# Kernel optimization log

Measured on AMD Instinct MI355X. Metric: run time of the kernel, lower is better.

Reference implementation:

```python
import jax, jax.numpy as jnp
import numpy as np

SPATIAL_SHAPES = ((100, 167), (50, 84), (25, 42), (13, 21))
NUM_HEADS = 8
NUM_LEVELS = 4
NUM_POINTS = 4
EMBED_DIM = 256
LV = sum(h * w for h, w in SPATIAL_SHAPES)  # 22223


def bilinear_sample(img, grid):
    """torch.F.grid_sample(mode='bilinear', padding_mode='zeros', align_corners=False).
    img: (B, D, H, W); grid: (B, Lq, P, 2) with xy in [-1, 1]. Returns (B, D, Lq, P)."""
    B, D, H, W = img.shape
    x = (grid[..., 0] + 1.0) * 0.5 * W - 0.5  # (B, Lq, P)
    y = (grid[..., 1] + 1.0) * 0.5 * H - 0.5
    x0 = jnp.floor(x)
    y0 = jnp.floor(y)
    wx1 = x - x0
    wy1 = y - y0
    wx0 = 1.0 - wx1
    wy0 = 1.0 - wy1

    def gather(ix, iy):
        valid = ((ix >= 0) & (ix <= W - 1) & (iy >= 0) & (iy <= H - 1)).astype(img.dtype)
        ixc = jnp.clip(ix, 0, W - 1).astype(jnp.int32)
        iyc = jnp.clip(iy, 0, H - 1).astype(jnp.int32)

        def g(img_b, ixb, iyb, vb):
            return img_b[:, iyb, ixb] * vb[None]  # (D, Lq, P)

        return jax.vmap(g)(img, ixc, iyc, valid)  # (B, D, Lq, P)

    v00 = gather(x0, y0)
    v01 = gather(x0 + 1, y0)
    v10 = gather(x0, y0 + 1)
    v11 = gather(x0 + 1, y0 + 1)
    w00 = (wy0 * wx0)[:, None]
    w01 = (wy0 * wx1)[:, None]
    w10 = (wy1 * wx0)[:, None]
    w11 = (wy1 * wx1)[:, None]
    return v00 * w00 + v01 * w01 + v10 * w10 + v11 * w11


def deform_attn(query, ref_points, value, W_off, b_off, W_attn, b_attn, W_val, b_val, W_out, b_out):
    N, Lq, C = query.shape
    D = C // NUM_HEADS
    off = (query @ W_off + b_off).reshape(N, Lq, NUM_HEADS, NUM_LEVELS, NUM_POINTS, 2)
    attn = jax.nn.softmax((query @ W_attn + b_attn).reshape(N, Lq, NUM_HEADS, NUM_LEVELS * NUM_POINTS), axis=-1)
    attn = attn.reshape(N, Lq, NUM_HEADS, NUM_LEVELS, NUM_POINTS)
    ref_cxcy = ref_points[:, :, None, :, None, :2]
    ref_wh = ref_points[:, :, None, :, None, 2:]
    loc = ref_cxcy + off / NUM_POINTS * ref_wh * 0.5
    grids = 2.0 * loc - 1.0  # (N, Lq, nh, L, P, 2)

    v = value @ W_val + b_val  # (N, Lv, C)
    sampled = []
    start = 0
    for lvl, (H, W) in enumerate(SPATIAL_SHAPES):
        v_l = v[:, start:start + H * W]  # (N, HW, C)
        start += H * W
        v_l = v_l.transpose(0, 2, 1).reshape(N * NUM_HEADS, D, H, W)
        g_l = grids[:, :, :, lvl].transpose(0, 2, 1, 3, 4).reshape(N * NUM_HEADS, Lq, NUM_POINTS, 2)
        sampled.append(bilinear_sample(v_l, g_l))  # (N*nh, D, Lq, P)
    sampled = jnp.concatenate(sampled, axis=-1)  # (N*nh, D, Lq, L*P)

    attn_r = attn.transpose(0, 2, 1, 3, 4).reshape(N * NUM_HEADS, 1, Lq, NUM_LEVELS * NUM_POINTS)
    out = (sampled * attn_r).sum(-1)  # (N*nh, D, Lq)
    out = out.reshape(N, C, Lq).transpose(0, 2, 1)
    return out @ W_out + b_out


def setup_inputs() -> dict:
    key = jax.random.key(0)
    ks = jax.random.split(key, 8)
    N, Lq, C = 1, LV, EMBED_DIM
    s = 0.02
    return {
        "query": jax.random.normal(ks[0], (N, Lq, C), jnp.float32),
        "ref_points": jax.random.uniform(ks[1], (N, Lq, NUM_LEVELS, 4), jnp.float32),
        "value": jax.random.normal(ks[2], (N, LV, C), jnp.float32),
        "W_off": jax.random.normal(ks[3], (C, NUM_HEADS * NUM_LEVELS * NUM_POINTS * 2), jnp.float32) * s,
        "b_off": jnp.zeros((NUM_HEADS * NUM_LEVELS * NUM_POINTS * 2,), jnp.float32),
        "W_attn": jax.random.normal(ks[4], (C, NUM_HEADS * NUM_LEVELS * NUM_POINTS), jnp.float32) * s,
        "b_attn": jnp.zeros((NUM_HEADS * NUM_LEVELS * NUM_POINTS,), jnp.float32),
        "W_val": jax.random.normal(ks[5], (C, C), jnp.float32) * s,
        "b_val": jnp.zeros((C,), jnp.float32),
        "W_out": jax.random.normal(ks[6], (C, C), jnp.float32) * s,
        "b_out": jnp.zeros((C,), jnp.float32),
    }


def reference(query, ref_points, value, W_off, b_off, W_attn, b_attn, W_val, b_val, W_out, b_out):
    return deform_attn(query, ref_points, value, W_off, b_off, W_attn, b_attn, W_val, b_val, W_out, b_out)
```

## Files before the change

### kernel.cpp

```cpp
#include <hip/hip_runtime.h>
#include <math.h>

#define LQ 22223
#define NH 8
#define NL 4
#define NP 4
#define CDIM 256
#define MBLK 348
#define NBV  (176 * 8)
#define NBOA (264 * 8)

typedef __attribute__((ext_vector_type(8))) short short8;
typedef __attribute__((ext_vector_type(4))) float f32x4;

__device__ __forceinline__ ushort f2bf(float f) {
    union { float f; unsigned u; } c; c.f = f;
    unsigned u = c.u;
    return (ushort)((u + 0x7fffu + ((u >> 16) & 1u)) >> 16);
}
__device__ __forceinline__ float bflo(unsigned u) {
    union { unsigned u; float f; } c; c.u = u << 16; return c.f;
}
__device__ __forceinline__ float bfhi(unsigned u) {
    union { unsigned u; float f; } c; c.u = u & 0xffff0000u; return c.f;
}

__global__ __launch_bounds__(256) void convert_wt(
    const float* __restrict__ Wv, const float* __restrict__ Wo,
    const float* __restrict__ Wu, const float* __restrict__ Wa,
    const float* __restrict__ bo, const float* __restrict__ ba,
    ushort* __restrict__ Tv, ushort* __restrict__ Toa,
    ushort* __restrict__ Tu, float* __restrict__ bcat)
{
    int idx = blockIdx.x * 256 + threadIdx.x;
    if (idx >= 229376) {
        int b = idx - 229376;
        if (b < 384) bcat[b] = (b < 256) ? bo[b] : ba[b - 256];
        return;
    }
    const float* W; ushort* T; int N; int local;
    if      (idx < 65536)  { W = Wv; T = Tv;          N = 256; local = idx; }
    else if (idx < 131072) { W = Wo; T = Toa;         N = 256; local = idx - 65536; }
    else if (idx < 196608) { W = Wu; T = Tu;          N = 256; local = idx - 131072; }
    else                   { W = Wa; T = Toa + 65536; N = 128; local = idx - 196608; }
    int k = local & 255;
    int n = local >> 8;
    T[n * 256 + k] = f2bf(W[k * N + n]);
}

__global__ __launch_bounds__(256, 5) void gemm_dual(
    const float* __restrict__ value, const ushort* __restrict__ Wtv,
    const float* __restrict__ bv, ushort* __restrict__ Cv,
    const float* __restrict__ query, const ushort* __restrict__ Wtoa,
    const float* __restrict__ boa, float* __restrict__ Coa)
{
    const int K = 256;
    __shared__ ushort As[2][64 * 40];
    __shared__ ushort Bs[2][64 * 40];

    int b = blockIdx.x;
    const float* A; const ushort* Bt; const float* bias;
    int N, bx, by; bool isv;
    const int xcd = b & 7;
    if (b < NBV) {
        isv = true;  A = value; Bt = Wtv;  bias = bv;  N = 256;
        const int j = b >> 3;
        bx = j & 3;  by = xcd + 8 * (j >> 2);
    } else {
        isv = false; A = query; Bt = Wtoa; bias = boa; N = 384;
        const int j = (b - NBV) >> 3;
        bx = j % 6;  by = xcd + 8 * (j / 6);
    }
    if (by >= MBLK) return;

    const int tid = threadIdx.x;
    const int w = tid >> 6;
    const int l = tid & 63;
    const int bm = by * 64;
    const int bn = bx * 64;

    const int r = tid >> 2;
    const int c = tid & 3;

    const int m_l  = (w << 4) + (l & 15);
    const int koff = (l >> 4) << 3;

    const bool arow_ok = (bm + r) < LQ;
    const float*  Ap = A  + (size_t)(bm + r) * K + c * 8;
    const ushort* Bp = Bt + (size_t)(bn + r) * K + c * 8;

    auto ldA = [&](int k0) -> short8 {
        short8 av = {0, 0, 0, 0, 0, 0, 0, 0};
        if (arow_ok) {
            const float4 f0 = *reinterpret_cast<const float4*>(Ap + k0);
            const float4 f1 = *reinterpret_cast<const float4*>(Ap + k0 + 4);
            av[0] = (short)f2bf(f0.x); av[1] = (short)f2bf(f0.y);
            av[2] = (short)f2bf(f0.z); av[3] = (short)f2bf(f0.w);
            av[4] = (short)f2bf(f1.x); av[5] = (short)f2bf(f1.y);
            av[6] = (short)f2bf(f1.z); av[7] = (short)f2bf(f1.w);
        }
        return av;
    };

    short8 av = ldA(0);
    short8 bvv = *reinterpret_cast<const short8*>(Bp);
    *reinterpret_cast<short8*>(&As[0][r * 40 + c * 8]) = av;
    *reinterpret_cast<short8*>(&Bs[0][r * 40 + c * 8]) = bvv;

    f32x4 acc[4] = {};

    #pragma unroll
    for (int k = 0; k < 8; ++k) {
        __syncthreads();
        if (k < 7) {
            av  = ldA((k + 1) * 32);
            bvv = *reinterpret_cast<const short8*>(Bp + (k + 1) * 32);
        }
        const int cur = k & 1;
        const short8 af = *reinterpret_cast<const short8*>(&As[cur][m_l * 40 + koff]);
        #pragma unroll
        for (int t = 0; t < 4; ++t) {
            const short8 bf = *reinterpret_cast<const short8*>(
                &Bs[cur][(t * 16 + (l & 15)) * 40 + koff]);
            acc[t] = __builtin_amdgcn_mfma_f32_16x16x32_bf16(af, bf, acc[t], 0, 0, 0);
        }
        if (k < 7) {
            const int nxt = cur ^ 1;
            *reinterpret_cast<short8*>(&As[nxt][r * 40 + c * 8]) = av;
            *reinterpret_cast<short8*>(&Bs[nxt][r * 40 + c * 8]) = bvv;
        }
    }

    const int row0 = bm + (w << 4) + ((l >> 4) << 2);
    #pragma unroll
    for (int t = 0; t < 4; ++t) {
        const int col = bn + t * 16 + (l & 15);
        const float bs = bias[col];
        #pragma unroll
        for (int i = 0; i < 4; ++i) {
            const int row = row0 + i;
            if (row < LQ) {
                const float o = acc[t][i] + bs;
                if (isv) {
                    const int head = col >> 5;
                    const int ch   = col & 31;
                    Cv[(size_t)head * ((size_t)LQ * 32) + (size_t)row * 32 + ch] = f2bf(o);
                } else {
                    Coa[(size_t)row * 384 + col] = o;
                }
            }
        }
    }
}

__global__ __launch_bounds__(256, 5) void gemm_out(
    const ushort* __restrict__ A, const ushort* __restrict__ Bt,
    const float* __restrict__ bias, float* __restrict__ C)
{
    const int K = 256, N = 256;
    __shared__ ushort As[2][64 * 40];
    __shared__ ushort Bs[2][64 * 40];

    const int b = blockIdx.x;
    const int xcd = b & 7;
    const int j = b >> 3;
    const int bx = j & 3;
    const int by = xcd + 8 * (j >> 2);
    if (by >= MBLK) return;

    const int tid = threadIdx.x;
    const int w = tid >> 6;
    const int l = tid & 63;
    const int bm = by * 64;
    const int bn = bx * 64;

    const int r = tid >> 2;
    const int c = tid & 3;

    const int m_l  = (w << 4) + (l & 15);
    const int koff = (l >> 4) << 3;

    const bool arow_ok = (bm + r) < LQ;
    const ushort* Ap = A  + (size_t)(bm + r) * K + c * 8;
    const ushort* Bp = Bt + (size_t)(bn + r) * K + c * 8;

    auto ldA = [&](int k0) -> short8 {
        short8 av = {0, 0, 0, 0, 0, 0, 0, 0};
        if (arow_ok) av = *reinterpret_cast<const short8*>(Ap + k0);
        return av;
    };

    short8 av = ldA(0);
    short8 bvv = *reinterpret_cast<const short8*>(Bp);
    *reinterpret_cast<short8*>(&As[0][r * 40 + c * 8]) = av;
    *reinterpret_cast<short8*>(&Bs[0][r * 40 + c * 8]) = bvv;

    f32x4 acc[4] = {};

    #pragma unroll
    for (int k = 0; k < 8; ++k) {
        __syncthreads();
        if (k < 7) {
            av  = ldA((k + 1) * 32);
            bvv = *reinterpret_cast<const short8*>(Bp + (k + 1) * 32);
        }
        const int cur = k & 1;
        const short8 af = *reinterpret_cast<const short8*>(&As[cur][m_l * 40 + koff]);
        #pragma unroll
        for (int t = 0; t < 4; ++t) {
            const short8 bf = *reinterpret_cast<const short8*>(
                &Bs[cur][(t * 16 + (l & 15)) * 40 + koff]);
            acc[t] = __builtin_amdgcn_mfma_f32_16x16x32_bf16(af, bf, acc[t], 0, 0, 0);
        }
        if (k < 7) {
            const int nxt = cur ^ 1;
            *reinterpret_cast<short8*>(&As[nxt][r * 40 + c * 8]) = av;
            *reinterpret_cast<short8*>(&Bs[nxt][r * 40 + c * 8]) = bvv;
        }
    }

    const int row0 = bm + (w << 4) + ((l >> 4) << 2);
    #pragma unroll
    for (int t = 0; t < 4; ++t) {
        const int col = bn + t * 16 + (l & 15);
        const float bs = bias[col];
        #pragma unroll
        for (int i = 0; i < 4; ++i) {
            const int row = row0 + i;
            if (row < LQ) C[(size_t)row * N + col] = acc[t][i] + bs;
        }
    }
}

__global__ __launch_bounds__(256) void softmax16(float* __restrict__ offattn, int rows)
{
    const int r = blockIdx.x * 256 + threadIdx.x;
    if (r >= rows) return;
    const int q = r >> 3;
    const int h = r & 7;
    float4* p = reinterpret_cast<float4*>(offattn + (size_t)q * 384 + 256 + h * 16);
    float v[16];
    #pragma unroll
    for (int i = 0; i < 4; ++i) {
        const float4 f = p[i];
        v[i * 4 + 0] = f.x; v[i * 4 + 1] = f.y; v[i * 4 + 2] = f.z; v[i * 4 + 3] = f.w;
    }
    float m = v[0];
    #pragma unroll
    for (int i = 1; i < 16; ++i) m = fmaxf(m, v[i]);
    float s = 0.f;
    #pragma unroll
    for (int i = 0; i < 16; ++i) { v[i] = expf(v[i] - m); s += v[i]; }
    const float inv = 1.f / s;
    #pragma unroll
    for (int i = 0; i < 4; ++i)
        p[i] = make_float4(v[i * 4 + 0] * inv, v[i * 4 + 1] * inv,
                           v[i * 4 + 2] * inv, v[i * 4 + 3] * inv);
}

__global__ __launch_bounds__(256, 4) void msda_sample(
    const ushort* __restrict__ v, const float* __restrict__ offattn,
    const float* __restrict__ ref, ushort* __restrict__ outp)
{
    __shared__ int4   s_off[512];
    __shared__ float4 s_wts[512];

    const int h = blockIdx.x & 7;
    const int qbase = (blockIdx.x >> 3) * 64;
    const int tid = threadIdx.x;

    const int Hs[4] = {100, 50, 25, 13};
    const int Ws[4] = {167, 84, 42, 21};
    const int starts[4] = {0, 16700, 20900, 21950};
    const int h32 = h * 32;

    const int qi = tid >> 2;
    const int dg = tid & 3;
    const int q2 = qbase + qi;
    const int d8 = dg * 8;
    const ushort* vh = v + (size_t)h * ((size_t)LQ * 32) + d8;

    float acc[8] = {};

    #pragma unroll
    for (int half = 0; half < 2; ++half) {
        if (half) __syncthreads();

        #pragma unroll
        for (int t2 = 0; t2 < 2; ++t2) {
            const int t = t2 * 256 + tid;
            const int qi1 = t & 63;
            const int pl = t >> 6;
            const int pi = half * 8 + pl;
            const int q = qbase + qi1;
            int4 ob = {0, 0, 0, 0};
            float4 wb = {0.f, 0.f, 0.f, 0.f};
            if (q < LQ) {
                const int l = pi >> 2;
                const int W = Ws[l], H = Hs[l];
                const float* refq = ref + (size_t)q * (NL * 4) + l * 4;
                const float cx = refq[0], cy = refq[1], rw = refq[2], rh = refq[3];
                const float* row = offattn + (size_t)q * 384;
                const float ox  = row[h32 + pi * 2];
                const float oy  = row[h32 + pi * 2 + 1];
                const float wgt = row[256 + h * 16 + pi];

                const float lx = cx + ox * 0.125f * rw;
                const float ly = cy + oy * 0.125f * rh;
                const float x = lx * (float)W - 0.5f;
                const float y = ly * (float)H - 0.5f;

                const float x0f = floorf(x);
                const float y0f = floorf(y);
                const int x0 = (int)x0f, y0 = (int)y0f;
                const float wx1 = x - x0f, wy1 = y - y0f;
                const float wx0 = 1.f - wx1, wy0 = 1.f - wy1;

                const bool xv0 = (x0 >= 0) && (x0 < W);
                const bool xv1 = (x0 + 1 >= 0) && (x0 + 1 < W);
                const bool yv0 = (y0 >= 0) && (y0 < H);
                const bool yv1 = (y0 + 1 >= 0) && (y0 + 1 < H);

                const int x0c = min(max(x0, 0), W - 1);
                const int x1c = min(max(x0 + 1, 0), W - 1);
                const int y0c = min(max(y0, 0), H - 1);
                const int y1c = min(max(y0 + 1, 0), H - 1);

                ob.x = (starts[l] + y0c * W + x0c) * 32;
                ob.y = (starts[l] + y0c * W + x1c) * 32;
                ob.z = (starts[l] + y1c * W + x0c) * 32;
                ob.w = (starts[l] + y1c * W + x1c) * 32;
                wb.x = (xv0 && yv0) ? wgt * wy0 * wx0 : 0.f;
                wb.y = (xv1 && yv0) ? wgt * wy0 * wx1 : 0.f;
                wb.z = (xv0 && yv1) ? wgt * wy1 * wx0 : 0.f;
                wb.w = (xv1 && yv1) ? wgt * wy1 * wx1 : 0.f;
            }
            s_off[t] = ob;
            s_wts[t] = wb;
        }
        __syncthreads();

        #pragma unroll 4
        for (int p = 0; p < 8; ++p) {
            const int4   o = s_off[p * 64 + qi];
            const float4 w = s_wts[p * 64 + qi];
            const uint4 a0 = *reinterpret_cast<const uint4*>(vh + o.x);
            const uint4 a1 = *reinterpret_cast<const uint4*>(vh + o.y);
            const uint4 a2 = *reinterpret_cast<const uint4*>(vh + o.z);
            const uint4 a3 = *reinterpret_cast<const uint4*>(vh + o.w);
            const unsigned u0[4] = {a0.x, a0.y, a0.z, a0.w};
            const unsigned u1[4] = {a1.x, a1.y, a1.z, a1.w};
            const unsigned u2[4] = {a2.x, a2.y, a2.z, a2.w};
            const unsigned u3[4] = {a3.x, a3.y, a3.z, a3.w};
            #pragma unroll
            for (int j = 0; j < 4; ++j) {
                acc[2 * j]     += w.x * bflo(u0[j]) + w.y * bflo(u1[j])
                                + w.z * bflo(u2[j]) + w.w * bflo(u3[j]);
                acc[2 * j + 1] += w.x * bfhi(u0[j]) + w.y * bfhi(u1[j])
                                + w.z * bfhi(u2[j]) + w.w * bfhi(u3[j]);
            }
        }
    }

    if (q2 < LQ) {
        short8 o8;
        #pragma unroll
        for (int j = 0; j < 8; ++j) o8[j] = (short)f2bf(acc[j]);
        *reinterpret_cast<short8*>(outp + (size_t)q2 * CDIM + h32 + d8) = o8;
    }
}

extern "C" void kernel_launch(void* const* d_in, const int* in_sizes, int n_in,
                              void* d_out, int out_size, void* d_ws, size_t ws_size,
                              hipStream_t stream)
{
    const float* query  = (const float*)d_in[0];
    const float* ref    = (const float*)d_in[1];
    const float* value  = (const float*)d_in[2];
    const float* W_off  = (const float*)d_in[3];
    const float* b_off  = (const float*)d_in[4];
    const float* W_attn = (const float*)d_in[5];
    const float* b_attn = (const float*)d_in[6];
    const float* W_val  = (const float*)d_in[7];
    const float* b_val  = (const float*)d_in[8];
    const float* W_out  = (const float*)d_in[9];
    const float* b_out  = (const float*)d_in[10];
    float* out = (float*)d_out;

    char* p = (char*)d_ws;
    ushort* v_bf    = (ushort*)p; p += (size_t)LQ * CDIM * 2;
    float*  offattn = (float*)p;  p += (size_t)LQ * 384 * 4;
    ushort* outp    = (ushort*)p; p += (size_t)LQ * CDIM * 2;
    ushort* Wt_val  = (ushort*)p; p += 65536 * 2;
    ushort* Wt_oa   = (ushort*)p; p += (65536 + 32768) * 2;
    ushort* Wt_out  = (ushort*)p; p += 65536 * 2;
    float*  bcat    = (float*)p;  p += 384 * 4;

    convert_wt<<<(229376 + 384 + 255) / 256, 256, 0, stream>>>(
        W_val, W_off, W_out, W_attn, b_off, b_attn, Wt_val, Wt_oa, Wt_out, bcat);

    gemm_dual<<<NBV + NBOA, 256, 0, stream>>>(
        value, Wt_val, b_val, v_bf, query, Wt_oa, bcat, offattn);

    softmax16<<<(LQ * NH + 255) / 256, 256, 0, stream>>>(offattn, LQ * NH);

    const int qg = (LQ + 63) / 64;
    msda_sample<<<qg * 8, 256, 0, stream>>>(v_bf, offattn, ref, outp);

    gemm_out<<<176 * 8, 256, 0, stream>>>(outp, Wt_out, b_out, out);
}
```

Measured before the change: 207.6 us.

## Enlarge GEMM tiles to 128x128 with 2x2 warp layout and 4x4 MFMA blocking

Both GEMM kernels move from 64x64 tiles, where each warp computes a 16x64 strip, to 128x128 tiles, where each warp computes a 64x64 sub-tile from four A and four B fragments. The goal is more MFMA work per LDS read and per global load, cutting redundant reloads of A and B. The grids shrink to match and launch bounds drop to 3 blocks per CU because of higher register and LDS use. Fewer blocks (352 for the value GEMM and for the output GEMM) means lower parallelism and occupancy, and may leave some CUs idle.

```diff
diff --git a/kernel.cpp b/kernel.cpp
--- a/kernel.cpp
+++ b/kernel.cpp
@@ -6,9 +6,10 @@
 #define NL 4
 #define NP 4
 #define CDIM 256
-#define MBLK 348
-#define NBV  (176 * 8)
-#define NBOA (264 * 8)
+#define MT 174
+#define NBV  (22 * 2 * 8)
+#define NBOA (22 * 3 * 8)
+#define NBO  (22 * 2 * 8)
 
 typedef __attribute__((ext_vector_type(8))) short short8;
 typedef __attribute__((ext_vector_type(4))) float f32x4;
@@ -23,6 +24,14 @@
 }
 __device__ __forceinline__ float bfhi(unsigned u) {
     union { unsigned u; float f; } c; c.u = u & 0xffff0000u; return c.f;
+}
+__device__ __forceinline__ short8 cvt8(float4 f0, float4 f1) {
+    short8 s;
+    s[0] = (short)f2bf(f0.x); s[1] = (short)f2bf(f0.y);
+    s[2] = (short)f2bf(f0.z); s[3] = (short)f2bf(f0.w);
+    s[4] = (short)f2bf(f1.x); s[5] = (short)f2bf(f1.y);
+    s[6] = (short)f2bf(f1.z); s[7] = (short)f2bf(f1.w);
+    return s;
 }
 
 __global__ __launch_bounds__(256) void convert_wt(
@@ -48,186 +57,220 @@
     T[n * 256 + k] = f2bf(W[k * N + n]);
 }
 
-__global__ __launch_bounds__(256, 5) void gemm_dual(
+__global__ __launch_bounds__(256, 3) void gemm_dual(
     const float* __restrict__ value, const ushort* __restrict__ Wtv,
     const float* __restrict__ bv, ushort* __restrict__ Cv,
     const float* __restrict__ query, const ushort* __restrict__ Wtoa,
     const float* __restrict__ boa, float* __restrict__ Coa)
 {
-    const int K = 256;
-    __shared__ ushort As[2][64 * 40];
-    __shared__ ushort Bs[2][64 * 40];
-
-    int b = blockIdx.x;
+    __shared__ ushort As[2][128 * 40];
+    __shared__ ushort Bs[2][128 * 40];
+
+    const int b = blockIdx.x;
     const float* A; const ushort* Bt; const float* bias;
-    int N, bx, by; bool isv;
+    int bx, by; bool isv;
     const int xcd = b & 7;
     if (b < NBV) {
-        isv = true;  A = value; Bt = Wtv;  bias = bv;  N = 256;
+        isv = true;  A = value; Bt = Wtv;  bias = bv;
         const int j = b >> 3;
-        bx = j & 3;  by = xcd + 8 * (j >> 2);
+        bx = j & 1;  by = xcd + 8 * (j >> 1);
     } else {
-        isv = false; A = query; Bt = Wtoa; bias = boa; N = 384;
+        isv = false; A = query; Bt = Wtoa; bias = boa;
         const int j = (b - NBV) >> 3;
-        bx = j % 6;  by = xcd + 8 * (j / 6);
-    }
-    if (by >= MBLK) return;
+        bx = j % 3;  by = xcd + 8 * (j / 3);
+    }
+    if (by >= MT) return;
 
     const int tid = threadIdx.x;
-    const int w = tid >> 6;
-    const int l = tid & 63;
-    const int bm = by * 64;
-    const int bn = bx * 64;
-
-    const int r = tid >> 2;
-    const int c = tid & 3;
-
-    const int m_l  = (w << 4) + (l & 15);
+    const int w  = tid >> 6;
+    const int l  = tid & 63;
+    const int wr = w >> 1, wc = w & 1;
+    const int bm = by * 128, bn = bx * 128;
+
+    const int r = tid >> 1;
+    const int c = tid & 1;
+
+    const int lm   = l & 15;
     const int koff = (l >> 4) << 3;
 
     const bool arow_ok = (bm + r) < LQ;
-    const float*  Ap = A  + (size_t)(bm + r) * K + c * 8;
-    const ushort* Bp = Bt + (size_t)(bn + r) * K + c * 8;
-
-    auto ldA = [&](int k0) -> short8 {
-        short8 av = {0, 0, 0, 0, 0, 0, 0, 0};
+    const float*  Ap = A  + (size_t)(bm + r) * 256 + c * 16;
+    const ushort* Bp = Bt + (size_t)(bn + r) * 256 + c * 16;
+
+    auto ldA = [&](int k0, short8& lo, short8& hi) {
+        lo = short8{0,0,0,0,0,0,0,0}; hi = short8{0,0,0,0,0,0,0,0};
         if (arow_ok) {
             const float4 f0 = *reinterpret_cast<const float4*>(Ap + k0);
             const float4 f1 = *reinterpret_cast<const float4*>(Ap + k0 + 4);
-            av[0] = (short)f2bf(f0.x); av[1] = (short)f2bf(f0.y);
-            av[2] = (short)f2bf(f0.z); av[3] = (short)f2bf(f0.w);
-            av[4] = (short)f2bf(f1.x); av[5] = (short)f2bf(f1.y);
-            av[6] = (short)f2bf(f1.z); av[7] = (short)f2bf(f1.w);
-        }
-        return av;
+            const float4 f2 = *reinterpret_cast<const float4*>(Ap + k0 + 8);
+            const float4 f3 = *reinterpret_cast<const float4*>(Ap + k0 + 12);
+            lo = cvt8(f0, f1); hi = cvt8(f2, f3);
+        }
     };
 
-    short8 av = ldA(0);
-    short8 bvv = *reinterpret_cast<const short8*>(Bp);
-    *reinterpret_cast<short8*>(&As[0][r * 40 + c * 8]) = av;
-    *reinterpret_cast<short8*>(&Bs[0][r * 40 + c * 8]) = bvv;
-
-    f32x4 acc[4] = {};
+    short8 a_lo, a_hi, b_lo, b_hi;
+    ldA(0, a_lo, a_hi);
+    b_lo = *reinterpret_cast<const short8*>(Bp);
+    b_hi = *reinterpret_cast<const short8*>(Bp + 8);
+    *reinterpret_cast<short8*>(&As[0][r * 40 + c * 16])     = a_lo;
+    *reinterpret_cast<short8*>(&As[0][r * 40 + c * 16 + 8]) = a_hi;
+    *reinterpret_cast<short8*>(&Bs[0][r * 40 + c * 16])     = b_lo;
+    *reinterpret_cast<short8*>(&Bs[0][r * 40 + c * 16 + 8]) = b_hi;
+
+    f32x4 acc[4][4] = {};
 
     #pragma unroll
     for (int k = 0; k < 8; ++k) {
         __syncthreads();
         if (k < 7) {
-            av  = ldA((k + 1) * 32);
-            bvv = *reinterpret_cast<const short8*>(Bp + (k + 1) * 32);
+            ldA((k + 1) * 32, a_lo, a_hi);
+            b_lo = *reinterpret_cast<const short8*>(Bp + (k + 1) * 32);
+            b_hi = *reinterpret_cast<const short8*>(Bp + (k + 1) * 32 + 8);
         }
         const int cur = k & 1;
-        const short8 af = *reinterpret_cast<const short8*>(&As[cur][m_l * 40 + koff]);
-        #pragma unroll
-        for (int t = 0; t < 4; ++t) {
-            const short8 bf = *reinterpret_cast<const short8*>(
-                &Bs[cur][(t * 16 + (l & 15)) * 40 + koff]);
-            acc[t] = __builtin_amdgcn_mfma_f32_16x16x32_bf16(af, bf, acc[t], 0, 0, 0);
-        }
+        short8 af[4], bf[4];
+        #pragma unroll
+        for (int m = 0; m < 4; ++m)
+            af[m] = *reinterpret_cast<const short8*>(
+                &As[cur][(wr * 64 + m * 16 + lm) * 40 + koff]);
+        #pragma unroll
+        for (int n = 0; n < 4; ++n)
+            bf[n] = *reinterpret_cast<const short8*>(
+                &Bs[cur][(wc * 64 + n * 16 + lm) * 40 + koff]);
+        #pragma unroll
+        for (int m = 0; m < 4; ++m)
+            #pragma unroll
+            for (int n = 0; n < 4; ++n)
+                acc[m][n] = __builtin_amdgcn_mfma_f32_16x16x32_bf16(
+                    af[m], bf[n], acc[m][n], 0, 0, 0);
         if (k < 7) {
             const int nxt = cur ^ 1;
-            *reinterpret_cast<short8*>(&As[nxt][r * 40 + c * 8]) = av;
-            *reinterpret_cast<short8*>(&Bs[nxt][r * 40 + c * 8]) = bvv;
-        }
-    }
-
-    const int row0 = bm + (w << 4) + ((l >> 4) << 2);
-    #pragma unroll
-    for (int t = 0; t < 4; ++t) {
-        const int col = bn + t * 16 + (l & 15);
-        const float bs = bias[col];
-        #pragma unroll
-        for (int i = 0; i < 4; ++i) {
-            const int row = row0 + i;
-            if (row < LQ) {
-                const float o = acc[t][i] + bs;
-                if (isv) {
-                    const int head = col >> 5;
-                    const int ch   = col & 31;
-                    Cv[(size_t)head * ((size_t)LQ * 32) + (size_t)row * 32 + ch] = f2bf(o);
-                } else {
-                    Coa[(size_t)row * 384 + col] = o;
+            *reinterpret_cast<short8*>(&As[nxt][r * 40 + c * 16])     = a_lo;
+            *reinterpret_cast<short8*>(&As[nxt][r * 40 + c * 16 + 8]) = a_hi;
+            *reinterpret_cast<short8*>(&Bs[nxt][r * 40 + c * 16])     = b_lo;
+            *reinterpret_cast<short8*>(&Bs[nxt][r * 40 + c * 16 + 8]) = b_hi;
+        }
+    }
+
+    const int row00 = bm + wr * 64 + ((l >> 4) << 2);
+    #pragma unroll
+    for (int m = 0; m < 4; ++m) {
+        #pragma unroll
+        for (int n = 0; n < 4; ++n) {
+            const int col = bn + wc * 64 + n * 16 + lm;
+            const float bs = bias[col];
+            #pragma unroll
+            for (int i = 0; i < 4; ++i) {
+                const int row = row00 + m * 16 + i;
+                if (row < LQ) {
+                    const float o = acc[m][n][i] + bs;
+                    if (isv) {
+                        const int head = col >> 5;
+                        const int ch   = col & 31;
+                        Cv[(size_t)head * ((size_t)LQ * 32) + (size_t)row * 32 + ch] = f2bf(o);
+                    } else {
+                        Coa[(size_t)row * 384 + col] = o;
+                    }
                 }
             }
         }
     }
 }
 
-__global__ __launch_bounds__(256, 5) void gemm_out(
+__global__ __launch_bounds__(256, 3) void gemm_out(
     const ushort* __restrict__ A, const ushort* __restrict__ Bt,
     const float* __restrict__ bias, float* __restrict__ C)
 {
-    const int K = 256, N = 256;
-    __shared__ ushort As[2][64 * 40];
-    __shared__ ushort Bs[2][64 * 40];
+    __shared__ ushort As[2][128 * 40];
+    __shared__ ushort Bs[2][128 * 40];
 
     const int b = blockIdx.x;
     const int xcd = b & 7;
     const int j = b >> 3;
-    const int bx = j & 3;
-    const int by = xcd + 8 * (j >> 2);
-    if (by >= MBLK) return;
+    const int bx = j & 1;
+    const int by = xcd + 8 * (j >> 1);
+    if (by >= MT) return;
 
     const int tid = threadIdx.x;
-    const int w = tid >> 6;
-    const int l = tid & 63;
-    const int bm = by * 64;
-    const int bn = bx * 64;
-
-    const int r = tid >> 2;
-    const int c = tid & 3;
-
-    const int m_l  = (w << 4) + (l & 15);
+    const int w  = tid >> 6;
+    const int l  = tid & 63;
+    const int wr = w >> 1, wc = w & 1;
+    const int bm = by * 128, bn = bx * 128;
+
+    const int r = tid >> 1;
+    const int c = tid & 1;
+
+    const int lm   = l & 15;
     const int koff = (l >> 4) << 3;
 
     const bool arow_ok = (bm + r) < LQ;
-    const ushort* Ap = A  + (size_t)(bm + r) * K + c * 8;
-    const ushort* Bp = Bt + (size_t)(bn + r) * K + c * 8;
-
-    auto ldA = [&](int k0) -> short8 {
-        short8 av = {0, 0, 0, 0, 0, 0, 0, 0};
-        if (arow_ok) av = *reinterpret_cast<const short8*>(Ap + k0);
-        return av;
+    const ushort* Ap = A  + (size_t)(bm + r) * 256 + c * 16;
+    const ushort* Bp = Bt + (size_t)(bn + r) * 256 + c * 16;
+
+    auto ldA = [&](int k0, short8& lo, short8& hi) {
+        lo = short8{0,0,0,0,0,0,0,0}; hi = short8{0,0,0,0,0,0,0,0};
+        if (arow_ok) {
+            lo = *reinterpret_cast<const short8*>(Ap + k0);
+            hi = *reinterpret_cast<const short8*>(Ap + k0 + 8);
+        }
     };
 
-    short8 av = ldA(0);
-    short8 bvv = *reinterpret_cast<const short8*>(Bp);
-    *reinterpret_cast<short8*>(&As[0][r * 40 + c * 8]) = av;
-    *reinterpret_cast<short8*>(&Bs[0][r * 40 + c * 8]) = bvv;
-
-    f32x4 acc[4] = {};
+    short8 a_lo, a_hi, b_lo, b_hi;
+    ldA(0, a_lo, a_hi);
+    b_lo = *reinterpret_cast<const short8*>(Bp);
+    b_hi = *reinterpret_cast<const short8*>(Bp + 8);
+    *reinterpret_cast<short8*>(&As[0][r * 40 + c * 16])     = a_lo;
+    *reinterpret_cast<short8*>(&As[0][r * 40 + c * 16 + 8]) = a_hi;
+    *reinterpret_cast<short8*>(&Bs[0][r * 40 + c * 16])     = b_lo;
+    *reinterpret_cast<short8*>(&Bs[0][r * 40 + c * 16 + 8]) = b_hi;
+
+    f32x4 acc[4][4] = {};
 
     #pragma unroll
     for (int k = 0; k < 8; ++k) {
         __syncthreads();
         if (k < 7) {
-            av  = ldA((k + 1) * 32);
-            bvv = *reinterpret_cast<const short8*>(Bp + (k + 1) * 32);
+            ldA((k + 1) * 32, a_lo, a_hi);
+            b_lo = *reinterpret_cast<const short8*>(Bp + (k + 1) * 32);
+            b_hi = *reinterpret_cast<const short8*>(Bp + (k + 1) * 32 + 8);
         }
         const int cur = k & 1;
-        const short8 af = *reinterpret_cast<const short8*>(&As[cur][m_l * 40 + koff]);
-        #pragma unroll
-        for (int t = 0; t < 4; ++t) {
-            const short8 bf = *reinterpret_cast<const short8*>(
-                &Bs[cur][(t * 16 + (l & 15)) * 40 + koff]);
-            acc[t] = __builtin_amdgcn_mfma_f32_16x16x32_bf16(af, bf, acc[t], 0, 0, 0);
-        }
+        short8 af[4], bf[4];
+        #pragma unroll
+        for (int m = 0; m < 4; ++m)
+            af[m] = *reinterpret_cast<const short8*>(
+                &As[cur][(wr * 64 + m * 16 + lm) * 40 + koff]);
+        #pragma unroll
+        for (int n = 0; n < 4; ++n)
+            bf[n] = *reinterpret_cast<const short8*>(
+                &Bs[cur][(wc * 64 + n * 16 + lm) * 40 + koff]);
+        #pragma unroll
+        for (int m = 0; m < 4; ++m)
+            #pragma unroll
+            for (int n = 0; n < 4; ++n)
+                acc[m][n] = __builtin_amdgcn_mfma_f32_16x16x32_bf16(
+                    af[m], bf[n], acc[m][n], 0, 0, 0);
         if (k < 7) {
             const int nxt = cur ^ 1;
-            *reinterpret_cast<short8*>(&As[nxt][r * 40 + c * 8]) = av;
-            *reinterpret_cast<short8*>(&Bs[nxt][r * 40 + c * 8]) = bvv;
-        }
-    }
-
-    const int row0 = bm + (w << 4) + ((l >> 4) << 2);
-    #pragma unroll
-    for (int t = 0; t < 4; ++t) {
-        const int col = bn + t * 16 + (l & 15);
-        const float bs = bias[col];
-        #pragma unroll
-        for (int i = 0; i < 4; ++i) {
-            const int row = row0 + i;
-            if (row < LQ) C[(size_t)row * N + col] = acc[t][i] + bs;
+            *reinterpret_cast<short8*>(&As[nxt][r * 40 + c * 16])     = a_lo;
+            *reinterpret_cast<short8*>(&As[nxt][r * 40 + c * 16 + 8]) = a_hi;
+            *reinterpret_cast<short8*>(&Bs[nxt][r * 40 + c * 16])     = b_lo;
+            *reinterpret_cast<short8*>(&Bs[nxt][r * 40 + c * 16 + 8]) = b_hi;
+        }
+    }
+
+    const int row00 = bm + wr * 64 + ((l >> 4) << 2);
+    #pragma unroll
+    for (int m = 0; m < 4; ++m) {
+        #pragma unroll
+        for (int n = 0; n < 4; ++n) {
+            const int col = bn + wc * 64 + n * 16 + lm;
+            const float bs = bias[col];
+            #pragma unroll
+            for (int i = 0; i < 4; ++i) {
+                const int row = row00 + m * 16 + i;
+                if (row < LQ) C[(size_t)row * 256 + col] = acc[m][n][i] + bs;
+            }
         }
     }
 }
@@ -407,5 +450,5 @@
     const int qg = (LQ + 63) / 64;
     msda_sample<<<qg * 8, 256, 0, stream>>>(v_bf, offattn, ref, outp);
 
-    gemm_out<<<176 * 8, 256, 0, stream>>>(outp, Wt_out, b_out, out);
-}
+    gemm_out<<<NBO, 256, 0, stream>>>(outp, Wt_out, b_out, out);
+}
```

New measurement: 211.2 us. Within noise of the previous version (+1.7%).

## Fuse softmax into GEMM epilogue and stage full-K tiles in LDS

Applied to the files above, without the earlier changes.

The separate softmax kernel is removed, and the attention-logit softmax now runs in the gemm_dual epilogue using 16-lane shuffle reductions over the per-head 16 columns. Both GEMMs now load the entire K=256 strip of A and B into LDS once with a single barrier, instead of double-buffering 32-wide K slices with a barrier per step. This drops one launch, one global read/write pass over the logits, and the per-step syncs. In exchange, LDS per block rises to about 67KB and launch bounds drop to 2 blocks per SM, which lowers occupancy and gives up the overlap of global loads with MFMA work.

```diff
diff --git a/kernel.cpp b/kernel.cpp
--- a/kernel.cpp
+++ b/kernel.cpp
@@ -9,6 +9,8 @@
 #define MBLK 348
 #define NBV  (176 * 8)
 #define NBOA (264 * 8)
+#define NBO  (176 * 8)
+#define LDSROW 264
 
 typedef __attribute__((ext_vector_type(8))) short short8;
 typedef __attribute__((ext_vector_type(4))) float f32x4;
@@ -48,26 +50,25 @@
     T[n * 256 + k] = f2bf(W[k * N + n]);
 }
 
-__global__ __launch_bounds__(256, 5) void gemm_dual(
+__global__ __launch_bounds__(256, 2) void gemm_dual(
     const float* __restrict__ value, const ushort* __restrict__ Wtv,
     const float* __restrict__ bv, ushort* __restrict__ Cv,
     const float* __restrict__ query, const ushort* __restrict__ Wtoa,
     const float* __restrict__ boa, float* __restrict__ Coa)
 {
-    const int K = 256;
-    __shared__ ushort As[2][64 * 40];
-    __shared__ ushort Bs[2][64 * 40];
-
-    int b = blockIdx.x;
+    __shared__ ushort As[64 * LDSROW];
+    __shared__ ushort Bs[64 * LDSROW];
+
+    const int b = blockIdx.x;
     const float* A; const ushort* Bt; const float* bias;
-    int N, bx, by; bool isv;
+    int bx, by; bool isv;
     const int xcd = b & 7;
     if (b < NBV) {
-        isv = true;  A = value; Bt = Wtv;  bias = bv;  N = 256;
+        isv = true;  A = value; Bt = Wtv;  bias = bv;
         const int j = b >> 3;
         bx = j & 3;  by = xcd + 8 * (j >> 2);
     } else {
-        isv = false; A = query; Bt = Wtoa; bias = boa; N = 384;
+        isv = false; A = query; Bt = Wtoa; bias = boa;
         const int j = (b - NBV) >> 3;
         bx = j % 6;  by = xcd + 8 * (j / 6);
     }
@@ -79,87 +80,107 @@
     const int bm = by * 64;
     const int bn = bx * 64;
 
-    const int r = tid >> 2;
-    const int c = tid & 3;
-
-    const int m_l  = (w << 4) + (l & 15);
-    const int koff = (l >> 4) << 3;
-
-    const bool arow_ok = (bm + r) < LQ;
-    const float*  Ap = A  + (size_t)(bm + r) * K + c * 8;
-    const ushort* Bp = Bt + (size_t)(bn + r) * K + c * 8;
-
-    auto ldA = [&](int k0) -> short8 {
-        short8 av = {0, 0, 0, 0, 0, 0, 0, 0};
-        if (arow_ok) {
-            const float4 f0 = *reinterpret_cast<const float4*>(Ap + k0);
-            const float4 f1 = *reinterpret_cast<const float4*>(Ap + k0 + 4);
-            av[0] = (short)f2bf(f0.x); av[1] = (short)f2bf(f0.y);
-            av[2] = (short)f2bf(f0.z); av[3] = (short)f2bf(f0.w);
-            av[4] = (short)f2bf(f1.x); av[5] = (short)f2bf(f1.y);
-            av[6] = (short)f2bf(f1.z); av[7] = (short)f2bf(f1.w);
-        }
-        return av;
-    };
-
-    short8 av = ldA(0);
-    short8 bvv = *reinterpret_cast<const short8*>(Bp);
-    *reinterpret_cast<short8*>(&As[0][r * 40 + c * 8]) = av;
-    *reinterpret_cast<short8*>(&Bs[0][r * 40 + c * 8]) = bvv;
+    {
+        const int rB = tid >> 5;
+        const int cB = (tid & 31) * 8;
+        #pragma unroll
+        for (int s = 0; s < 8; ++s) {
+            const int row = s * 8 + rB;
+            const short8 v8 = *reinterpret_cast<const short8*>(
+                Bt + (size_t)(bn + row) * 256 + cB);
+            *reinterpret_cast<short8*>(&Bs[row * LDSROW + cB]) = v8;
+        }
+    }
+    {
+        const int rA = tid >> 6;
+        const int cA = (tid & 63) * 4;
+        #pragma unroll
+        for (int s = 0; s < 16; ++s) {
+            const int row = s * 4 + rA;
+            unsigned lo = 0, hi = 0;
+            if (bm + row < LQ) {
+                const float4 f = *reinterpret_cast<const float4*>(
+                    A + (size_t)(bm + row) * 256 + cA);
+                lo = (unsigned)f2bf(f.x) | ((unsigned)f2bf(f.y) << 16);
+                hi = (unsigned)f2bf(f.z) | ((unsigned)f2bf(f.w) << 16);
+            }
+            uint2 p; p.x = lo; p.y = hi;
+            *reinterpret_cast<uint2*>(&As[row * LDSROW + cA]) = p;
+        }
+    }
+
+    __syncthreads();
+
+    const int lm  = l & 15;
+    const int j4  = l >> 4;
+    const int m_l = (w << 4) + lm;
 
     f32x4 acc[4] = {};
-
     #pragma unroll
-    for (int k = 0; k < 8; ++k) {
-        __syncthreads();
-        if (k < 7) {
-            av  = ldA((k + 1) * 32);
-            bvv = *reinterpret_cast<const short8*>(Bp + (k + 1) * 32);
-        }
-        const int cur = k & 1;
-        const short8 af = *reinterpret_cast<const short8*>(&As[cur][m_l * 40 + koff]);
+    for (int kk = 0; kk < 8; ++kk) {
+        const int ko = kk * 32 + j4 * 8;
+        const short8 af = *reinterpret_cast<const short8*>(&As[m_l * LDSROW + ko]);
         #pragma unroll
         for (int t = 0; t < 4; ++t) {
             const short8 bf = *reinterpret_cast<const short8*>(
-                &Bs[cur][(t * 16 + (l & 15)) * 40 + koff]);
+                &Bs[(t * 16 + lm) * LDSROW + ko]);
             acc[t] = __builtin_amdgcn_mfma_f32_16x16x32_bf16(af, bf, acc[t], 0, 0, 0);
         }
-        if (k < 7) {
-            const int nxt = cur ^ 1;
-            *reinterpret_cast<short8*>(&As[nxt][r * 40 + c * 8]) = av;
-            *reinterpret_cast<short8*>(&Bs[nxt][r * 40 + c * 8]) = bvv;
-        }
-    }
-
-    const int row0 = bm + (w << 4) + ((l >> 4) << 2);
-    #pragma unroll
-    for (int t = 0; t < 4; ++t) {
-        const int col = bn + t * 16 + (l & 15);
-        const float bs = bias[col];
-        #pragma unroll
-        for (int i = 0; i < 4; ++i) {
-            const int row = row0 + i;
-            if (row < LQ) {
-                const float o = acc[t][i] + bs;
-                if (isv) {
-                    const int head = col >> 5;
-                    const int ch   = col & 31;
-                    Cv[(size_t)head * ((size_t)LQ * 32) + (size_t)row * 32 + ch] = f2bf(o);
-                } else {
-                    Coa[(size_t)row * 384 + col] = o;
+    }
+
+    const int row0 = bm + (w << 4) + (j4 << 2);
+
+    if (!isv && bx >= 4) {
+        #pragma unroll
+        for (int t = 0; t < 4; ++t) {
+            const int col = bn + t * 16 + lm;
+            const float bs = bias[col];
+            #pragma unroll
+            for (int i = 0; i < 4; ++i) {
+                const int row = row0 + i;
+                const float L = acc[t][i] + bs;
+                float mx = L;
+                #pragma unroll
+                for (int s = 1; s < 16; s <<= 1)
+                    mx = fmaxf(mx, __shfl_xor(mx, s));
+                const float e = expf(L - mx);
+                float sum = e;
+                #pragma unroll
+                for (int s = 1; s < 16; s <<= 1)
+                    sum += __shfl_xor(sum, s);
+                if (row < LQ)
+                    Coa[(size_t)row * 384 + col] = e / sum;
+            }
+        }
+    } else {
+        #pragma unroll
+        for (int t = 0; t < 4; ++t) {
+            const int col = bn + t * 16 + lm;
+            const float bs = bias[col];
+            #pragma unroll
+            for (int i = 0; i < 4; ++i) {
+                const int row = row0 + i;
+                if (row < LQ) {
+                    const float o = acc[t][i] + bs;
+                    if (isv) {
+                        const int head = col >> 5;
+                        const int ch   = col & 31;
+                        Cv[(size_t)head * ((size_t)LQ * 32) + (size_t)row * 32 + ch] = f2bf(o);
+                    } else {
+                        Coa[(size_t)row * 384 + col] = o;
+                    }
                 }
             }
         }
     }
 }
 
-__global__ __launch_bounds__(256, 5) void gemm_out(
+__global__ __launch_bounds__(256, 2) void gemm_out(
     const ushort* __restrict__ A, const ushort* __restrict__ Bt,
     const float* __restrict__ bias, float* __restrict__ C)
 {
-    const int K = 256, N = 256;
-    __shared__ ushort As[2][64 * 40];
-    __shared__ ushort Bs[2][64 * 40];
+    __shared__ ushort As[64 * LDSROW];
+    __shared__ ushort Bs[64 * LDSROW];
 
     const int b = blockIdx.x;
     const int xcd = b & 7;
@@ -174,88 +195,54 @@
     const int bm = by * 64;
     const int bn = bx * 64;
 
-    const int r = tid >> 2;
-    const int c = tid & 3;
-
-    const int m_l  = (w << 4) + (l & 15);
-    const int koff = (l >> 4) << 3;
-
-    const bool arow_ok = (bm + r) < LQ;
-    const ushort* Ap = A  + (size_t)(bm + r) * K + c * 8;
-    const ushort* Bp = Bt + (size_t)(bn + r) * K + c * 8;
-
-    auto ldA = [&](int k0) -> short8 {
-        short8 av = {0, 0, 0, 0, 0, 0, 0, 0};
-        if (arow_ok) av = *reinterpret_cast<const short8*>(Ap + k0);
-        return av;
-    };
-
-    short8 av = ldA(0);
-    short8 bvv = *reinterpret_cast<const short8*>(Bp);
-    *reinterpret_cast<short8*>(&As[0][r * 40 + c * 8]) = av;
-    *reinterpret_cast<short8*>(&Bs[0][r * 40 + c * 8]) = bvv;
+    {
+        const int rB = tid >> 5;
+        const int cB = (tid & 31) * 8;
+        #pragma unroll
+        for (int s = 0; s < 8; ++s) {
+            const int row = s * 8 + rB;
+            const short8 v8 = *reinterpret_cast<const short8*>(
+                Bt + (size_t)(bn + row) * 256 + cB);
+            *reinterpret_cast<short8*>(&Bs[row * LDSROW + cB]) = v8;
+
+            short8 a8 = {0, 0, 0, 0, 0, 0, 0, 0};
+            if (bm + row < LQ)
+                a8 = *reinterpret_cast<const short8*>(
+                    A + (size_t)(bm + row) * 256 + cB);
+            *reinterpret_cast<short8*>(&As[row * LDSROW + cB]) = a8;
+        }
+    }
+
+    __syncthreads();
+
+    const int lm  = l & 15;
+    const int j4  = l >> 4;
+    const int m_l = (w << 4) + lm;
 
     f32x4 acc[4] = {};
-
     #pragma unroll
-    for (int k = 0; k < 8; ++k) {
-        __syncthreads();
-        if (k < 7) {
-            av  = ldA((k + 1) * 32);
-            bvv = *reinterpret_cast<const short8*>(Bp + (k + 1) * 32);
-        }
-        const int cur = k & 1;
-        const short8 af = *reinterpret_cast<const short8*>(&As[cur][m_l * 40 + koff]);
+    for (int kk = 0; kk < 8; ++kk) {
+        const int ko = kk * 32 + j4 * 8;
+        const short8 af = *reinterpret_cast<const short8*>(&As[m_l * LDSROW + ko]);
         #pragma unroll
         for (int t = 0; t < 4; ++t) {
             const short8 bf = *reinterpret_cast<const short8*>(
-                &Bs[cur][(t * 16 + (l & 15)) * 40 + koff]);
+                &Bs[(t * 16 + lm) * LDSROW + ko]);
             acc[t] = __builtin_amdgcn_mfma_f32_16x16x32_bf16(af, bf, acc[t], 0, 0, 0);
         }
-        if (k < 7) {
-            const int nxt = cur ^ 1;
-            *reinterpret_cast<short8*>(&As[nxt][r * 40 + c * 8]) = av;
-            *reinterpret_cast<short8*>(&Bs[nxt][r * 40 + c * 8]) = bvv;
-        }
-    }
-
-    const int row0 = bm + (w << 4) + ((l >> 4) << 2);
+    }
+
+    const int row0 = bm + (w << 4) + (j4 << 2);
     #pragma unroll
     for (int t = 0; t < 4; ++t) {
-        const int col = bn + t * 16 + (l & 15);
+        const int col = bn + t * 16 + lm;
         const float bs = bias[col];
         #pragma unroll
         for (int i = 0; i < 4; ++i) {
             const int row = row0 + i;
-            if (row < LQ) C[(size_t)row * N + col] = acc[t][i] + bs;
-        }
-    }
-}
-
-__global__ __launch_bounds__(256) void softmax16(float* __restrict__ offattn, int rows)
-{
-    const int r = blockIdx.x * 256 + threadIdx.x;
-    if (r >= rows) return;
-    const int q = r >> 3;
-    const int h = r & 7;
-    float4* p = reinterpret_cast<float4*>(offattn + (size_t)q * 384 + 256 + h * 16);
-    float v[16];
-    #pragma unroll
-    for (int i = 0; i < 4; ++i) {
-        const float4 f = p[i];
-        v[i * 4 + 0] = f.x; v[i * 4 + 1] = f.y; v[i * 4 + 2] = f.z; v[i * 4 + 3] = f.w;
-    }
-    float m = v[0];
-    #pragma unroll
-    for (int i = 1; i < 16; ++i) m = fmaxf(m, v[i]);
-    float s = 0.f;
-    #pragma unroll
-    for (int i = 0; i < 16; ++i) { v[i] = expf(v[i] - m); s += v[i]; }
-    const float inv = 1.f / s;
-    #pragma unroll
-    for (int i = 0; i < 4; ++i)
-        p[i] = make_float4(v[i * 4 + 0] * inv, v[i * 4 + 1] * inv,
-                           v[i * 4 + 2] * inv, v[i * 4 + 3] * inv);
+            if (row < LQ) C[(size_t)row * 256 + col] = acc[t][i] + bs;
+        }
+    }
 }
 
 __global__ __launch_bounds__(256, 4) void msda_sample(
@@ -402,10 +389,8 @@
     gemm_dual<<<NBV + NBOA, 256, 0, stream>>>(
         value, Wt_val, b_val, v_bf, query, Wt_oa, bcat, offattn);
 
-    softmax16<<<(LQ * NH + 255) / 256, 256, 0, stream>>>(offattn, LQ * NH);
-
     const int qg = (LQ + 63) / 64;
     msda_sample<<<qg * 8, 256, 0, stream>>>(v_bf, offattn, ref, outp);
 
-    gemm_out<<<176 * 8, 256, 0, stream>>>(outp, Wt_out, b_out, out);
-}
+    gemm_out<<<NBO, 256, 0, stream>>>(outp, Wt_out, b_out, out);
+}
```

Result: slower. 251.4 us (+21.1%).
